# Optimization experiments

Hardware: AMD Instinct MI355X
Metric: run time of the kernel (lower is better)

## Reference

```python
import jax, jax.numpy as jnp
import numpy as np

D = 1024
N = 8192

def setup_inputs() -> dict:
    key = jax.random.key(0)
    ks = jax.random.split(key, 9)
    s = 1.0 / np.sqrt(D)
    return {
        "queries": jax.random.normal(ks[0], (N, D), dtype=jnp.float32),
        "key": jax.random.normal(ks[1], (N, D), dtype=jnp.float32),
        "values": jax.random.normal(ks[2], (N, D), dtype=jnp.float32),
        "Wq": jax.random.normal(ks[3], (D, D), dtype=jnp.float32) * s,
        "bq": jnp.zeros((D,), dtype=jnp.float32),
        "Wk": jax.random.normal(ks[4], (D, D), dtype=jnp.float32) * s,
        "bk": jnp.zeros((D,), dtype=jnp.float32),
        "Wv": jax.random.normal(ks[5], (D, D), dtype=jnp.float32) * s,
        "bv": jnp.zeros((D,), dtype=jnp.float32),
    }

def reference(queries, key, values, Wq, bq, Wk, bk, Wv, bv):
    # Linear layers: x @ W^T + b (torch nn.Linear convention)
    q = queries @ Wq.T + bq          # [N, D]
    k = key @ Wk.T + bk              # [N, D]
    v = values @ Wv.T + bv           # [N, D]
    scale = 1.0 / jnp.sqrt(jnp.asarray(float(q.shape[-1]), dtype=q.dtype))
    scores = (q @ k.T) * scale       # [N, N]
    p = jax.nn.softmax(scores, axis=-1)  # legacy nn.Softmax() on 2D -> dim=1
    return p @ v                     # [N, D]
```

## Files before the change

### kernel.cpp

```cpp
#include <hip/hip_runtime.h>
#include <hip/hip_bf16.h>
#include <stdint.h>

#define NN 8192
#define DD 1024

typedef __attribute__((ext_vector_type(4))) float f32x4;
typedef __attribute__((ext_vector_type(8))) short bf16x8;
using bf16_t = __hip_bfloat16;

__device__ __forceinline__ void gload16(const void* g, void* l) {
  __builtin_amdgcn_global_load_lds(
      (const __attribute__((address_space(1))) void*)g,
      (__attribute__((address_space(3))) void*)l, 16, 0, 0);
}

__global__ __launch_bounds__(256) void cast_bf16_kernel(
    const float* __restrict__ in, bf16_t* __restrict__ out, int n8) {
  int i = blockIdx.x * 256 + threadIdx.x;
  if (i >= n8) return;
  const float4* p4 = (const float4*)in + (size_t)i * 2;
  float4 a = p4[0], b = p4[1];
  __align__(16) bf16_t tmp[8];
  tmp[0] = __float2bfloat16(a.x); tmp[1] = __float2bfloat16(a.y);
  tmp[2] = __float2bfloat16(a.z); tmp[3] = __float2bfloat16(a.w);
  tmp[4] = __float2bfloat16(b.x); tmp[5] = __float2bfloat16(b.y);
  tmp[6] = __float2bfloat16(b.z); tmp[7] = __float2bfloat16(b.w);
  *((uint4*)out + i) = *(const uint4*)tmp;
}

template<int MODE>
__global__ __launch_bounds__(256, 2)
void gemm_bt(const bf16_t* __restrict__ A, const bf16_t* __restrict__ B,
             const float* __restrict__ bias, void* __restrict__ Cout,
             float* __restrict__ aux,
             int M, int Nc, int K, int ldc, float scale, int nbx) {
  __shared__ bf16_t As[128 * 32];
  __shared__ bf16_t Bs[128 * 32];
  __shared__ float rsum[128];
  const int t = threadIdx.x;
  const int nwg = gridDim.x;
  const int bid = (blockIdx.x & 7) * (nwg >> 3) + (blockIdx.x >> 3);
  const int bm = bid / nbx, bn = bid % nbx;
  const int lane = t & 63, wave = t >> 6;
  const int wr = wave >> 1, wc = wave & 1;

  const int c0 = t, c1 = t + 256;
  const bf16_t* ag0 = A + (size_t)(bm * 128 + (c0 >> 2)) * K + (c0 & 3) * 8;
  const bf16_t* ag1 = A + (size_t)(bm * 128 + (c1 >> 2)) * K + (c1 & 3) * 8;
  const bf16_t* bg0 = B + (size_t)(bn * 128 + (c0 >> 2)) * K + (c0 & 3) * 8;
  const bf16_t* bg1 = B + (size_t)(bn * 128 + (c1 >> 2)) * K + (c1 & 3) * 8;
  bf16_t* la0 = As + c0 * 8;
  bf16_t* la1 = As + c1 * 8;
  bf16_t* lb0 = Bs + c0 * 8;
  bf16_t* lb1 = Bs + c1 * 8;

  f32x4 acc[4][4] = {};
  const int fr = lane & 15;
  const int ko = (lane >> 4) * 8;

  for (int kt = 0; kt < K; kt += 32) {
    gload16(ag0 + kt, la0);
    gload16(ag1 + kt, la1);
    gload16(bg0 + kt, lb0);
    gload16(bg1 + kt, lb1);
    __syncthreads();
    bf16x8 af[4], bf[4];
#pragma unroll
    for (int m = 0; m < 4; m++)
      af[m] = *(const bf16x8*)&As[(wr * 64 + m * 16 + fr) * 32 + ko];
#pragma unroll
    for (int n = 0; n < 4; n++)
      bf[n] = *(const bf16x8*)&Bs[(wc * 64 + n * 16 + fr) * 32 + ko];
#pragma unroll
    for (int m = 0; m < 4; m++)
#pragma unroll
      for (int n = 0; n < 4; n++)
        acc[m][n] = __builtin_amdgcn_mfma_f32_16x16x32_bf16(af[m], bf[n], acc[m][n], 0, 0, 0);
    __syncthreads();
  }

  const int rb = (lane >> 4) * 4;

  if (MODE == 3) {
    if (t < 128) rsum[t] = 0.f;
    __syncthreads();
  }

  float rs[4][4];
#pragma unroll
  for (int m = 0; m < 4; m++)
#pragma unroll
    for (int j = 0; j < 4; j++) rs[m][j] = 0.f;

#pragma unroll
  for (int m = 0; m < 4; m++) {
#pragma unroll
    for (int n = 0; n < 4; n++) {
      const int col = bn * 128 + wc * 64 + n * 16 + fr;
      const int row0 = bm * 128 + wr * 64 + m * 16 + rb;
      if (MODE == 0) {
        bf16_t* C = (bf16_t*)Cout;
        const float bv = bias[col];
#pragma unroll
        for (int j = 0; j < 4; j++)
          C[(size_t)(row0 + j) * ldc + col] = __float2bfloat16((acc[m][n][j] + bv) * scale);
      } else if (MODE == 1) {
        bf16_t* C = (bf16_t*)Cout;
        const float bv = bias[col];
        __align__(8) bf16_t tmp[4];
#pragma unroll
        for (int j = 0; j < 4; j++)
          tmp[j] = __float2bfloat16((acc[m][n][j] + bv) * scale);
        *(ushort4*)&C[(size_t)col * ldc + row0] = *(const ushort4*)tmp;
      } else if (MODE == 3) {
        bf16_t* C = (bf16_t*)Cout;
#pragma unroll
        for (int j = 0; j < 4; j++) {
          float e = exp2f(acc[m][n][j] * 1.44269504088896f);
          bf16_t pb = __float2bfloat16(e);
          C[(size_t)(row0 + j) * ldc + col] = pb;
          rs[m][j] += __bfloat162float(pb);
        }
      } else {
        float* C = (float*)Cout;
#pragma unroll
        for (int j = 0; j < 4; j++)
          C[(size_t)(row0 + j) * ldc + col] = acc[m][n][j] * aux[row0 + j];
      }
    }
  }

  if (MODE == 3) {
#pragma unroll
    for (int m = 0; m < 4; m++) {
#pragma unroll
      for (int j = 0; j < 4; j++) {
        float v = rs[m][j];
        v += __shfl_xor(v, 1);
        v += __shfl_xor(v, 2);
        v += __shfl_xor(v, 4);
        v += __shfl_xor(v, 8);
        if (fr == 0) atomicAdd(&rsum[wr * 64 + m * 16 + rb + j], v);
      }
    }
    __syncthreads();
    if (t < 128) aux[(size_t)bn * M + bm * 128 + t] = rsum[t];
  }
}

__global__ __launch_bounds__(256) void rowsum_inv_kernel(
    const float* __restrict__ partial, float* __restrict__ inv_l, int nb) {
  const int r = blockIdx.x * 256 + threadIdx.x;
  float s = 0.f;
  for (int b = 0; b < nb; b++) s += partial[(size_t)b * NN + r];
  inv_l[r] = 1.f / s;
}

extern "C" void kernel_launch(void* const* d_in, const int* in_sizes, int n_in,
                              void* d_out, int out_size, void* d_ws, size_t ws_size,
                              hipStream_t stream) {
  const float* queries = (const float*)d_in[0];
  const float* key_in  = (const float*)d_in[1];
  const float* values  = (const float*)d_in[2];
  const float* Wq = (const float*)d_in[3];
  const float* bq = (const float*)d_in[4];
  const float* Wk = (const float*)d_in[5];
  const float* bk = (const float*)d_in[6];
  const float* Wv = (const float*)d_in[7];
  const float* bv = (const float*)d_in[8];
  float* out = (float*)d_out;
  char* ws = (char*)d_ws;

  const size_t MB = 1024 * 1024;

  bf16_t* qb = (bf16_t*)(ws);
  bf16_t* kb = (bf16_t*)(ws + 16 * MB);
  bf16_t* vT = (bf16_t*)(ws + 32 * MB);
  bf16_t* P  = (bf16_t*)(ws + 48 * MB);
  float* partial = (float*)(ws + 176 * MB);
  float* inv_l   = (float*)(ws + 178 * MB);
  bf16_t* xb = (bf16_t*)(ws + 48 * MB);
  bf16_t* wb = (bf16_t*)(ws + 64 * MB);

  const int nd8 = NN * DD / 8, dd8 = DD * DD / 8;

  cast_bf16_kernel<<<nd8 / 256, 256, 0, stream>>>(queries, xb, nd8);
  cast_bf16_kernel<<<dd8 / 256, 256, 0, stream>>>(Wq, wb, dd8);
  gemm_bt<0><<<(NN / 128) * (DD / 128), 256, 0, stream>>>(
      xb, wb, bq, qb, nullptr, NN, DD, DD, DD, 0.03125f, DD / 128);
  cast_bf16_kernel<<<nd8 / 256, 256, 0, stream>>>(key_in, xb, nd8);
  cast_bf16_kernel<<<dd8 / 256, 256, 0, stream>>>(Wk, wb, dd8);
  gemm_bt<0><<<(NN / 128) * (DD / 128), 256, 0, stream>>>(
      xb, wb, bk, kb, nullptr, NN, DD, DD, DD, 1.0f, DD / 128);
  cast_bf16_kernel<<<nd8 / 256, 256, 0, stream>>>(values, xb, nd8);
  cast_bf16_kernel<<<dd8 / 256, 256, 0, stream>>>(Wv, wb, dd8);
  gemm_bt<1><<<(NN / 128) * (DD / 128), 256, 0, stream>>>(
      xb, wb, bv, vT, nullptr, NN, DD, DD, NN, 1.0f, DD / 128);

  gemm_bt<3><<<(NN / 128) * (NN / 128), 256, 0, stream>>>(
      qb, kb, nullptr, P, partial, NN, NN, DD, NN, 1.0f, NN / 128);
  rowsum_inv_kernel<<<NN / 256, 256, 0, stream>>>(partial, inv_l, NN / 128);
  gemm_bt<4><<<(NN / 128) * (DD / 128), 256, 0, stream>>>(
      P, vT, nullptr, out, inv_l, NN, DD, NN, DD, 1.0f, DD / 128);
}
```

Measured before the change: 483.2 us.

## Use 256x256 pipelined double-buffered GEMM with split-K for attention matmuls

Adds a new 512-thread GEMM kernel with 256x256 tiles, a 64-wide K step, swizzled LDS, double-buffered direct-to-LDS loads interleaved with MFMA phases, and setprio scheduling. It is used for the QK^T+exp stage and for the PV stage. The PV stage runs as a 2-way split-K, and a new combine kernel adds the two partials and applies the row normalization. The aim is higher MFMA utilization and less LDS/global traffic per FLOP, at the cost of more LDS use, an extra partial buffer and an extra elementwise pass.

```diff
diff --git a/kernel.cpp b/kernel.cpp
--- a/kernel.cpp
+++ b/kernel.cpp
@@ -14,6 +14,7 @@
       (const __attribute__((address_space(1))) void*)g,
       (__attribute__((address_space(3))) void*)l, 16, 0, 0);
 }
+__device__ __forceinline__ int imin(int a, int b) { return a < b ? a : b; }
 
 __global__ __launch_bounds__(256) void cast_bf16_kernel(
     const float* __restrict__ in, bf16_t* __restrict__ out, int n8) {
@@ -33,11 +34,9 @@
 __global__ __launch_bounds__(256, 2)
 void gemm_bt(const bf16_t* __restrict__ A, const bf16_t* __restrict__ B,
              const float* __restrict__ bias, void* __restrict__ Cout,
-             float* __restrict__ aux,
              int M, int Nc, int K, int ldc, float scale, int nbx) {
   __shared__ bf16_t As[128 * 32];
   __shared__ bf16_t Bs[128 * 32];
-  __shared__ float rsum[128];
   const int t = threadIdx.x;
   const int nwg = gridDim.x;
   const int bid = (blockIdx.x & 7) * (nwg >> 3) + (blockIdx.x >> 3);
@@ -65,34 +64,22 @@
     gload16(bg0 + kt, lb0);
     gload16(bg1 + kt, lb1);
     __syncthreads();
-    bf16x8 af[4], bf[4];
+    bf16x8 af[4], bfv[4];
 #pragma unroll
     for (int m = 0; m < 4; m++)
       af[m] = *(const bf16x8*)&As[(wr * 64 + m * 16 + fr) * 32 + ko];
 #pragma unroll
     for (int n = 0; n < 4; n++)
-      bf[n] = *(const bf16x8*)&Bs[(wc * 64 + n * 16 + fr) * 32 + ko];
+      bfv[n] = *(const bf16x8*)&Bs[(wc * 64 + n * 16 + fr) * 32 + ko];
 #pragma unroll
     for (int m = 0; m < 4; m++)
 #pragma unroll
       for (int n = 0; n < 4; n++)
-        acc[m][n] = __builtin_amdgcn_mfma_f32_16x16x32_bf16(af[m], bf[n], acc[m][n], 0, 0, 0);
+        acc[m][n] = __builtin_amdgcn_mfma_f32_16x16x32_bf16(af[m], bfv[n], acc[m][n], 0, 0, 0);
     __syncthreads();
   }
 
   const int rb = (lane >> 4) * 4;
-
-  if (MODE == 3) {
-    if (t < 128) rsum[t] = 0.f;
-    __syncthreads();
-  }
-
-  float rs[4][4];
-#pragma unroll
-  for (int m = 0; m < 4; m++)
-#pragma unroll
-    for (int j = 0; j < 4; j++) rs[m][j] = 0.f;
-
 #pragma unroll
   for (int m = 0; m < 4; m++) {
 #pragma unroll
@@ -105,7 +92,7 @@
 #pragma unroll
         for (int j = 0; j < 4; j++)
           C[(size_t)(row0 + j) * ldc + col] = __float2bfloat16((acc[m][n][j] + bv) * scale);
-      } else if (MODE == 1) {
+      } else {
         bf16_t* C = (bf16_t*)Cout;
         const float bv = bias[col];
         __align__(8) bf16_t tmp[4];
@@ -113,40 +100,178 @@
         for (int j = 0; j < 4; j++)
           tmp[j] = __float2bfloat16((acc[m][n][j] + bv) * scale);
         *(ushort4*)&C[(size_t)col * ldc + row0] = *(const ushort4*)tmp;
-      } else if (MODE == 3) {
-        bf16_t* C = (bf16_t*)Cout;
-#pragma unroll
-        for (int j = 0; j < 4; j++) {
-          float e = exp2f(acc[m][n][j] * 1.44269504088896f);
-          bf16_t pb = __float2bfloat16(e);
-          C[(size_t)(row0 + j) * ldc + col] = pb;
-          rs[m][j] += __bfloat162float(pb);
-        }
-      } else {
-        float* C = (float*)Cout;
-#pragma unroll
-        for (int j = 0; j < 4; j++)
-          C[(size_t)(row0 + j) * ldc + col] = acc[m][n][j] * aux[row0 + j];
       }
     }
   }
+}
+
+template<int MODE>
+__global__ __launch_bounds__(512, 2)
+void gemm256(const bf16_t* __restrict__ A, int lda,
+             const bf16_t* __restrict__ B, int ldb,
+             void* __restrict__ Cout, int ldc,
+             float* __restrict__ aux, int ksplit, int nkt, int nbx, int Mrows) {
+  __shared__ char smem_raw[131072];
+  const int t = threadIdx.x;
+  const int nwg = gridDim.x;
+  const int bid = (blockIdx.x & 7) * (nwg >> 3) + (blockIdx.x >> 3);
+  const int bm = bid / nbx, bn = bid % nbx;
+  const int lane = t & 63, wave = t >> 6;
+  const int wr = wave >> 2, wc = wave & 3;
+  const int fr = lane & 15, hi = lane >> 4;
+  const int k0 = blockIdx.y * ksplit;
+
+  const int cswz = ((t & 7) ^ (((t >> 5) & 1) << 1)) * 8;
+  uint32_t offA[2][2], offB[2][2];
+#pragma unroll
+  for (int h = 0; h < 2; h++)
+#pragma unroll
+    for (int l = 0; l < 2; l++) {
+      const int r = h * 128 + l * 64 + (t >> 3);
+      offA[h][l] = (uint32_t)((bm * 256 + r) * lda + k0 + cswz);
+      offB[h][l] = (uint32_t)((bn * 256 + r) * ldb + k0 + cswz);
+    }
+
+  const int xsw = ((fr >> 2) & 1) << 5;
+  const int rdA0 = (((wr * 128 + fr) * 128) + hi * 16) ^ xsw;
+  const int rdB0 = ((((wc * 64 + fr) * 128) + hi * 16) ^ xsw) + 32768;
+
+  f32x4 acc[8][4] = {};
+  bf16x8 af[4][2], bl[2][2], bh[2][2];
+
+#define STA(buf, h, kt)                                                        \
+  gload16(A + offA[h][0] + (size_t)(kt) * 64,                                  \
+          smem_raw + (buf) * 65536 + (h) * 16384 + t * 16);                    \
+  gload16(A + offA[h][1] + (size_t)(kt) * 64,                                  \
+          smem_raw + (buf) * 65536 + (h) * 16384 + 8192 + t * 16);
+#define STB(buf, h, kt)                                                        \
+  gload16(B + offB[h][0] + (size_t)(kt) * 64,                                  \
+          smem_raw + (buf) * 65536 + 32768 + (h) * 16384 + t * 16);            \
+  gload16(B + offB[h][1] + (size_t)(kt) * 64,                                  \
+          smem_raw + (buf) * 65536 + 32768 + (h) * 16384 + 8192 + t * 16);
+#define RDA(buf, mf, ks) \
+  (*(const bf16x8*)(smem_raw + (buf) * 65536 + rdA0 + (mf) * 2048 + (ks) * 64))
+#define RDB(buf, nf, ks) \
+  (*(const bf16x8*)(smem_raw + (buf) * 65536 + rdB0 + (nf) * 2048 + (ks) * 64))
+#define MFMA8(BF, m0, n0)                                                      \
+  _Pragma("unroll") for (int m = 0; m < 4; m++)                                \
+  _Pragma("unroll") for (int n = 0; n < 2; n++)                                \
+  _Pragma("unroll") for (int ks = 0; ks < 2; ks++)                             \
+    acc[(m0) + m][(n0) + n] = __builtin_amdgcn_mfma_f32_16x16x32_bf16(         \
+        af[m][ks], BF[n][ks], acc[(m0) + m][(n0) + n], 0, 0, 0);
+#define MIDSYNC()                                                              \
+  __builtin_amdgcn_s_barrier();                                                \
+  asm volatile("s_waitcnt lgkmcnt(0)" ::: "memory");                           \
+  __builtin_amdgcn_sched_barrier(0);
+
+  STB(0, 0, 0) STB(0, 1, 0) STA(0, 0, 0) STA(0, 1, 0)
+  STB(1, 0, 1) STB(1, 1, 1)
+  asm volatile("s_waitcnt vmcnt(4)" ::: "memory");
+  __builtin_amdgcn_s_barrier();
+
+  const int nit = nkt >> 1;
+  for (int it = 0; it < nit; ++it) {
+    const int T1 = 2 * it + 1;
+    const int s2 = imin(2 * it + 2, nkt - 1);
+    const int s3 = imin(2 * it + 3, nkt - 1);
+#pragma unroll
+    for (int m = 0; m < 4; m++) { af[m][0] = RDA(0, m, 0); af[m][1] = RDA(0, m, 1); }
+#pragma unroll
+    for (int n = 0; n < 2; n++) { bl[n][0] = RDB(0, n, 0); bl[n][1] = RDB(0, n, 1); }
+    STA(1, 0, T1)
+    MIDSYNC();
+    __builtin_amdgcn_s_setprio(1); MFMA8(bl, 0, 0) __builtin_amdgcn_s_setprio(0);
+    __builtin_amdgcn_s_barrier();
+#pragma unroll
+    for (int n = 0; n < 2; n++) { bh[n][0] = RDB(0, 2 + n, 0); bh[n][1] = RDB(0, 2 + n, 1); }
+    STA(1, 1, T1)
+    MIDSYNC();
+    __builtin_amdgcn_s_setprio(1); MFMA8(bh, 0, 2) __builtin_amdgcn_s_setprio(0);
+    __builtin_amdgcn_s_barrier();
+#pragma unroll
+    for (int m = 0; m < 4; m++) { af[m][0] = RDA(0, 4 + m, 0); af[m][1] = RDA(0, 4 + m, 1); }
+    STB(0, 0, s2)
+    MIDSYNC();
+    __builtin_amdgcn_s_setprio(1); MFMA8(bh, 4, 2) __builtin_amdgcn_s_setprio(0);
+    __builtin_amdgcn_s_barrier();
+    STB(0, 1, s2)
+    MIDSYNC();
+    __builtin_amdgcn_s_setprio(1); MFMA8(bl, 4, 0) __builtin_amdgcn_s_setprio(0);
+    asm volatile("s_waitcnt vmcnt(4)" ::: "memory");
+    __builtin_amdgcn_s_barrier();
+#pragma unroll
+    for (int m = 0; m < 4; m++) { af[m][0] = RDA(1, m, 0); af[m][1] = RDA(1, m, 1); }
+#pragma unroll
+    for (int n = 0; n < 2; n++) { bl[n][0] = RDB(1, n, 0); bl[n][1] = RDB(1, n, 1); }
+    STA(0, 0, s2)
+    MIDSYNC();
+    __builtin_amdgcn_s_setprio(1); MFMA8(bl, 0, 0) __builtin_amdgcn_s_setprio(0);
+    __builtin_amdgcn_s_barrier();
+#pragma unroll
+    for (int n = 0; n < 2; n++) { bh[n][0] = RDB(1, 2 + n, 0); bh[n][1] = RDB(1, 2 + n, 1); }
+    STA(0, 1, s2)
+    MIDSYNC();
+    __builtin_amdgcn_s_setprio(1); MFMA8(bh, 0, 2) __builtin_amdgcn_s_setprio(0);
+    __builtin_amdgcn_s_barrier();
+#pragma unroll
+    for (int m = 0; m < 4; m++) { af[m][0] = RDA(1, 4 + m, 0); af[m][1] = RDA(1, 4 + m, 1); }
+    STB(1, 0, s3)
+    MIDSYNC();
+    __builtin_amdgcn_s_setprio(1); MFMA8(bh, 4, 2) __builtin_amdgcn_s_setprio(0);
+    __builtin_amdgcn_s_barrier();
+    STB(1, 1, s3)
+    MIDSYNC();
+    __builtin_amdgcn_s_setprio(1); MFMA8(bl, 4, 0) __builtin_amdgcn_s_setprio(0);
+    asm volatile("s_waitcnt vmcnt(4)" ::: "memory");
+    __builtin_amdgcn_s_barrier();
+  }
+
+  asm volatile("s_waitcnt vmcnt(0)" ::: "memory");
+  __builtin_amdgcn_s_barrier();
+
+  const int gr0 = bm * 256 + wr * 128 + hi * 4;
+  const int gc0 = bn * 256 + wc * 64 + fr;
 
   if (MODE == 3) {
-#pragma unroll
-    for (int m = 0; m < 4; m++) {
+    float* rsum = (float*)smem_raw;
+    if (t < 256) rsum[t] = 0.f;
+    __syncthreads();
+    bf16_t* C = (bf16_t*)Cout;
+#pragma unroll
+    for (int mf = 0; mf < 8; mf++) {
 #pragma unroll
       for (int j = 0; j < 4; j++) {
-        float v = rs[m][j];
-        v += __shfl_xor(v, 1);
-        v += __shfl_xor(v, 2);
-        v += __shfl_xor(v, 4);
-        v += __shfl_xor(v, 8);
-        if (fr == 0) atomicAdd(&rsum[wr * 64 + m * 16 + rb + j], v);
+        float rs = 0.f;
+#pragma unroll
+        for (int nf = 0; nf < 4; nf++) {
+          float e = exp2f(acc[mf][nf][j] * 1.44269504088896f);
+          bf16_t pb = __float2bfloat16(e);
+          C[(size_t)(gr0 + mf * 16 + j) * ldc + gc0 + nf * 16] = pb;
+          rs += __bfloat162float(pb);
+        }
+        rs += __shfl_xor(rs, 1); rs += __shfl_xor(rs, 2);
+        rs += __shfl_xor(rs, 4); rs += __shfl_xor(rs, 8);
+        if (fr == 0) atomicAdd(&rsum[wr * 128 + mf * 16 + hi * 4 + j], rs);
       }
     }
     __syncthreads();
-    if (t < 128) aux[(size_t)bn * M + bm * 128 + t] = rsum[t];
+    if (t < 256) aux[(size_t)bn * Mrows + bm * 256 + t] = rsum[t];
+  } else {
+    float* C = blockIdx.y == 0 ? (float*)Cout : aux;
+#pragma unroll
+    for (int mf = 0; mf < 8; mf++)
+#pragma unroll
+      for (int nf = 0; nf < 4; nf++)
+#pragma unroll
+        for (int j = 0; j < 4; j++)
+          C[(size_t)(gr0 + mf * 16 + j) * ldc + gc0 + nf * 16] = acc[mf][nf][j];
   }
+#undef STA
+#undef STB
+#undef RDA
+#undef RDB
+#undef MFMA8
+#undef MIDSYNC
 }
 
 __global__ __launch_bounds__(256) void rowsum_inv_kernel(
@@ -155,6 +280,18 @@
   float s = 0.f;
   for (int b = 0; b < nb; b++) s += partial[(size_t)b * NN + r];
   inv_l[r] = 1.f / s;
+}
+
+__global__ __launch_bounds__(256) void combine_kernel(
+    float* __restrict__ out, const float* __restrict__ o1,
+    const float* __restrict__ inv_l) {
+  const size_t i = (size_t)blockIdx.x * 256 + threadIdx.x;
+  const float s = inv_l[(int)((i * 4) >> 10)];
+  float4 a = ((const float4*)out)[i];
+  const float4 b = ((const float4*)o1)[i];
+  a.x = (a.x + b.x) * s; a.y = (a.y + b.y) * s;
+  a.z = (a.z + b.z) * s; a.w = (a.w + b.w) * s;
+  ((float4*)out)[i] = a;
 }
 
 extern "C" void kernel_launch(void* const* d_in, const int* in_sizes, int n_in,
@@ -173,13 +310,13 @@
   char* ws = (char*)d_ws;
 
   const size_t MB = 1024 * 1024;
-
   bf16_t* qb = (bf16_t*)(ws);
   bf16_t* kb = (bf16_t*)(ws + 16 * MB);
   bf16_t* vT = (bf16_t*)(ws + 32 * MB);
   bf16_t* P  = (bf16_t*)(ws + 48 * MB);
   float* partial = (float*)(ws + 176 * MB);
-  float* inv_l   = (float*)(ws + 178 * MB);
+  float* inv_l   = (float*)(ws + 177 * MB);
+  float* o1      = (float*)(ws + 178 * MB);
   bf16_t* xb = (bf16_t*)(ws + 48 * MB);
   bf16_t* wb = (bf16_t*)(ws + 64 * MB);
 
@@ -188,19 +325,20 @@
   cast_bf16_kernel<<<nd8 / 256, 256, 0, stream>>>(queries, xb, nd8);
   cast_bf16_kernel<<<dd8 / 256, 256, 0, stream>>>(Wq, wb, dd8);
   gemm_bt<0><<<(NN / 128) * (DD / 128), 256, 0, stream>>>(
-      xb, wb, bq, qb, nullptr, NN, DD, DD, DD, 0.03125f, DD / 128);
+      xb, wb, bq, qb, NN, DD, DD, DD, 0.03125f, DD / 128);
   cast_bf16_kernel<<<nd8 / 256, 256, 0, stream>>>(key_in, xb, nd8);
   cast_bf16_kernel<<<dd8 / 256, 256, 0, stream>>>(Wk, wb, dd8);
   gemm_bt<0><<<(NN / 128) * (DD / 128), 256, 0, stream>>>(
-      xb, wb, bk, kb, nullptr, NN, DD, DD, DD, 1.0f, DD / 128);
+      xb, wb, bk, kb, NN, DD, DD, DD, 1.0f, DD / 128);
   cast_bf16_kernel<<<nd8 / 256, 256, 0, stream>>>(values, xb, nd8);
   cast_bf16_kernel<<<dd8 / 256, 256, 0, stream>>>(Wv, wb, dd8);
   gemm_bt<1><<<(NN / 128) * (DD / 128), 256, 0, stream>>>(
-      xb, wb, bv, vT, nullptr, NN, DD, DD, NN, 1.0f, DD / 128);
-
-  gemm_bt<3><<<(NN / 128) * (NN / 128), 256, 0, stream>>>(
-      qb, kb, nullptr, P, partial, NN, NN, DD, NN, 1.0f, NN / 128);
-  rowsum_inv_kernel<<<NN / 256, 256, 0, stream>>>(partial, inv_l, NN / 128);
-  gemm_bt<4><<<(NN / 128) * (DD / 128), 256, 0, stream>>>(
-      P, vT, nullptr, out, inv_l, NN, DD, NN, DD, 1.0f, DD / 128);
-}
+      xb, wb, bv, vT, NN, DD, DD, NN, 1.0f, DD / 128);
+
+  gemm256<3><<<dim3((NN / 256) * (NN / 256)), 512, 0, stream>>>(
+      qb, DD, kb, DD, P, NN, partial, 0, DD / 64, NN / 256, NN);
+  rowsum_inv_kernel<<<NN / 256, 256, 0, stream>>>(partial, inv_l, NN / 256);
+  gemm256<4><<<dim3((NN / 256) * (DD / 256), 2), 512, 0, stream>>>(
+      P, NN, vT, NN, out, DD, o1, NN / 2, NN / 2 / 64, DD / 256, NN);
+  combine_kernel<<<NN * DD / 4 / 256, 256, 0, stream>>>(out, o1, inv_l);
+}
```

Measured after the change: 425.2 us. 1.14x faster.
